# Optimization experiments

Measured on AMD Instinct MI355X. Metric: run time of the kernel, lower is better.

Reference implementation:

```python
import jax, jax.numpy as jnp
import numpy as np

DIM = 1024
N_HEADS = 16
HEAD_DIM = DIM // N_HEADS
B, S = 2, 2048
NEG = -1e9  # additive causal mask value (finite, safe in low precision)


def setup_inputs() -> dict:
    key = jax.random.key(0)
    k_x, k_q, k_k, k_v, k_o = jax.random.split(key, 5)
    x = jax.random.normal(k_x, (B, S, DIM), dtype=jnp.float32)
    # causal additive mask, broadcastable to [B, H, S, S]
    causal = jnp.triu(jnp.ones((S, S), dtype=bool), k=1)
    mask = jnp.where(causal, NEG, 0.0).astype(jnp.float32)[None, None]
    scale = 1.0 / np.sqrt(DIM)
    wq = jax.random.normal(k_q, (DIM, DIM), dtype=jnp.float32) * scale
    wk = jax.random.normal(k_k, (DIM, DIM), dtype=jnp.float32) * scale
    wv = jax.random.normal(k_v, (DIM, DIM), dtype=jnp.float32) * scale
    wo = jax.random.normal(k_o, (DIM, DIM), dtype=jnp.float32) * scale
    return {"x": x, "mask": mask, "wq": wq, "wk": wk, "wv": wv, "wo": wo}


def reference(x, mask, wq, wk, wv, wo):
    bs, seqlen, _ = x.shape
    # nn.Linear(y) = y @ W^T ; weights stored as (out, in)
    q = (x @ wq.T).reshape(bs, seqlen, N_HEADS, HEAD_DIM)
    k = (x @ wk.T).reshape(bs, seqlen, N_HEADS, HEAD_DIM)
    v = (x @ wv.T).reshape(bs, seqlen, N_HEADS, HEAD_DIM)
    # scores: [B, H, S, S] — intentionally materialized, as in the original
    attn = jnp.einsum('bqhd,bkhd->bhqk', q, k) / np.sqrt(HEAD_DIM)
    attn = attn + mask
    attn = jax.nn.softmax(attn, axis=-1)
    out = jnp.einsum('bhqk,bkhd->bqhd', attn, v).reshape(bs, seqlen, DIM)
    return out @ wo.T
```

## Files before the change

### kernel.cpp

```cpp
#include <hip/hip_runtime.h>

typedef __attribute__((ext_vector_type(8))) short bf16x8;
typedef __attribute__((ext_vector_type(4))) float f32x4;
typedef __attribute__((ext_vector_type(16))) float f32x16;
typedef __attribute__((ext_vector_type(4))) unsigned short u16x4;
typedef __attribute__((ext_vector_type(8))) unsigned short u16x8;

#define DIM 1024
#define SEQ 2048
#define NHEAD 16
#define HDIM 64
#define C2 0.18033688011112042f
#define KFIX 8.0f

__device__ __forceinline__ unsigned short f2bf(float f) {
  union { float f; unsigned u; } v; v.f = f;
  unsigned r = v.u + 0x7fffu + ((v.u >> 16) & 1u);
  return (unsigned short)(r >> 16);
}

__device__ __forceinline__ float bf2f(unsigned short s) {
  union { unsigned u; float f; } v; v.u = ((unsigned)s) << 16;
  return v.f;
}

__device__ __forceinline__ void gload_lds16(const void* g, void* l) {
  __builtin_amdgcn_global_load_lds(
      (const __attribute__((address_space(1))) void*)g,
      (__attribute__((address_space(3))) void*)l, 16, 0, 0);
}

__device__ __forceinline__ f32x16 mfma32(bf16x8 a, bf16x8 b, f32x16 c) {
  return __builtin_amdgcn_mfma_f32_32x32x16_bf16(a, b, c, 0, 0, 0);
}

__device__ __forceinline__ unsigned cvtpk(float lo, float hi) {
  unsigned r;
  asm("v_cvt_pk_bf16_f32 %0, %1, %2" : "=v"(r) : "v"(lo), "v"(hi));
  return r;
}

__global__ void f2bf_all(const float* __restrict__ x, const float* __restrict__ wq,
                         const float* __restrict__ wk, const float* __restrict__ wv,
                         const float* __restrict__ wo, unsigned short* __restrict__ xb,
                         unsigned short* __restrict__ wb) {
  int blk = blockIdx.x;
  const float* src;
  unsigned short* dst;
  int rb;
  if (blk < 4096) { src = x; dst = xb; rb = blk; }
  else {
    int w = (blk - 4096) >> 10;
    src = w == 0 ? wq : w == 1 ? wk : w == 2 ? wv : wo;
    dst = wb + (size_t)w * 1048576;
    rb = (blk - 4096) & 1023;
  }
  int i = rb * 256 + threadIdx.x;
  float4 v = ((const float4*)src)[i];
  u16x4 o;
  o[0] = f2bf(v.x); o[1] = f2bf(v.y); o[2] = f2bf(v.z); o[3] = f2bf(v.w);
  ((u16x4*)dst)[i] = o;
}

__global__ __launch_bounds__(256) void gemm3(
    const unsigned short* __restrict__ xb,
    const unsigned short* __restrict__ wb,
    unsigned short* __restrict__ qkv) {
  __shared__ unsigned short As[2][8192];
  __shared__ unsigned short Bs[2][8192];
  const int bz = blockIdx.x;
  const unsigned short *A, *B;
  unsigned short* C;
  int m0, n0, ldc;
  float cscale = 1.0f;
  if (bz < 512) {
    int xcd = bz & 7, inner = bz >> 3;
    int mm = inner & 3, n = (inner >> 2) & 7, w = inner >> 5;
    m0 = (xcd * 4 + mm) * 128; n0 = n * 128;
    A = xb; B = wb + w * 1048576; C = qkv + w * 4194304; ldc = 1024;
    if (w == 0) cscale = C2;
  } else {
    int idx = bz - 512;
    int xcd = idx & 7, inner = idx >> 3;
    int tt = inner & 3, mv = inner >> 2;
    m0 = mv * 128; n0 = (xcd * 4 + tt) * 128;
    A = wb + 2 * 1048576; B = xb; C = qkv + 2 * 4194304; ldc = 4096;
  }
  const int tid = threadIdx.x;
  const int wv = tid >> 6, lane = tid & 63;
  const int g = lane >> 4, l16 = lane & 15;
  const int wm = (wv >> 1) * 64, wn = (wv & 1) * 64;
  f32x4 acc[4][4] = {};

#define GSTAGE(IT, BUF)                                                        \
  {                                                                            \
    const int kt = (IT) * 64;                                                  \
    _Pragma("unroll")                                                          \
    for (int qq = 0; qq < 4; ++qq) {                                           \
      int rbase = wv * 32 + qq * 8;                                            \
      int r = rbase + (lane >> 3);                                             \
      int cs = ((lane & 7) ^ (r & 7)) * 8;                                     \
      gload_lds16(A + (long long)(m0 + r) * 1024 + kt + cs,                    \
                  &As[BUF][rbase * 64]);                                       \
      gload_lds16(B + (long long)(n0 + r) * 1024 + kt + cs,                    \
                  &Bs[BUF][rbase * 64]);                                       \
    }                                                                          \
  }

  GSTAGE(0, 0);
  __syncthreads();

  for (int it = 0; it < 16; ++it) {
    const int buf = it & 1;
    if (it + 1 < 16) GSTAGE(it + 1, buf ^ 1);
#pragma unroll
    for (int ks = 0; ks < 2; ++ks) {
      bf16x8 af[4], bfr[4];
      const int cb = ks * 64 + g * 16;
#pragma unroll
      for (int mf = 0; mf < 4; ++mf) {
        int row = wm + mf * 16 + l16;
        af[mf] = *(const bf16x8*)((const char*)&As[buf][0] + row * 128 + (cb ^ ((row & 7) << 4)));
      }
#pragma unroll
      for (int nf = 0; nf < 4; ++nf) {
        int row = wn + nf * 16 + l16;
        bfr[nf] = *(const bf16x8*)((const char*)&Bs[buf][0] + row * 128 + (cb ^ ((row & 7) << 4)));
      }
#pragma unroll
      for (int mf = 0; mf < 4; ++mf)
#pragma unroll
        for (int nf = 0; nf < 4; ++nf)
          acc[mf][nf] = __builtin_amdgcn_mfma_f32_16x16x32_bf16(
              af[mf], bfr[nf], acc[mf][nf], 0, 0, 0);
    }
    __syncthreads();
  }

#pragma unroll
  for (int mf = 0; mf < 4; ++mf)
#pragma unroll
    for (int nf = 0; nf < 4; ++nf)
#pragma unroll
      for (int r = 0; r < 4; ++r) {
        long long m = m0 + wm + mf * 16 + g * 4 + r;
        long long n = n0 + wn + nf * 16 + l16;
        C[m * ldc + n] = f2bf(acc[mf][nf][r] * cscale);
      }
}

__global__ __launch_bounds__(256) void gemm_out(
    const unsigned short* __restrict__ A,
    const unsigned short* __restrict__ B,
    float* __restrict__ C) {
  __shared__ unsigned short As[2][8192];
  __shared__ unsigned short Bs[2][8192];
  const int tid = threadIdx.x;
  const int wv = tid >> 6, lane = tid & 63;
  const int g = lane >> 4, l16 = lane & 15;
  const int m0 = blockIdx.y * 128, n0 = blockIdx.x * 128;
  const int wm = (wv >> 1) * 64, wn = (wv & 1) * 64;
  f32x4 acc[4][4] = {};

#define OSTAGE(IT, BUF)                                                        \
  {                                                                            \
    const int kt = (IT) * 64;                                                  \
    _Pragma("unroll")                                                          \
    for (int qq = 0; qq < 4; ++qq) {                                           \
      int rbase = wv * 32 + qq * 8;                                            \
      int r = rbase + (lane >> 3);                                             \
      int cs = ((lane & 7) ^ (r & 7)) * 8;                                     \
      gload_lds16(A + (long long)(m0 + r) * 1024 + kt + cs,                    \
                  &As[BUF][rbase * 64]);                                       \
      gload_lds16(B + (long long)(n0 + r) * 1024 + kt + cs,                    \
                  &Bs[BUF][rbase * 64]);                                       \
    }                                                                          \
  }

  OSTAGE(0, 0);
  __syncthreads();

  for (int it = 0; it < 16; ++it) {
    const int buf = it & 1;
    if (it + 1 < 16) OSTAGE(it + 1, buf ^ 1);
#pragma unroll
    for (int ks = 0; ks < 2; ++ks) {
      bf16x8 af[4], bfr[4];
      const int cb = ks * 64 + g * 16;
#pragma unroll
      for (int mf = 0; mf < 4; ++mf) {
        int row = wm + mf * 16 + l16;
        af[mf] = *(const bf16x8*)((const char*)&As[buf][0] + row * 128 + (cb ^ ((row & 7) << 4)));
      }
#pragma unroll
      for (int nf = 0; nf < 4; ++nf) {
        int row = wn + nf * 16 + l16;
        bfr[nf] = *(const bf16x8*)((const char*)&Bs[buf][0] + row * 128 + (cb ^ ((row & 7) << 4)));
      }
#pragma unroll
      for (int mf = 0; mf < 4; ++mf)
#pragma unroll
        for (int nf = 0; nf < 4; ++nf)
          acc[mf][nf] = __builtin_amdgcn_mfma_f32_16x16x32_bf16(
              af[mf], bfr[nf], acc[mf][nf], 0, 0, 0);
    }
    __syncthreads();
  }

#pragma unroll
  for (int mf = 0; mf < 4; ++mf)
#pragma unroll
    for (int nf = 0; nf < 4; ++nf)
#pragma unroll
      for (int r = 0; r < 4; ++r) {
        long long m = m0 + wm + mf * 16 + g * 4 + r;
        long long n = n0 + wn + nf * 16 + l16;
        C[m * 1024 + n] = acc[mf][nf][r];
      }
}

__global__ __launch_bounds__(256, 3) void attn_kernel(
    const unsigned short* __restrict__ Qg,
    const unsigned short* __restrict__ Kg,
    const unsigned short* __restrict__ VTg,
    unsigned short* __restrict__ Og,
    unsigned short* __restrict__ pacc,
    float* __restrict__ pml) {
  __shared__ unsigned short Kls[2][4096];
  __shared__ unsigned short Vls[2][4096];

  const int tid = threadIdx.x;
  const int wv = tid >> 6, lane = tid & 63;
  const int l32 = lane & 31, hi = lane >> 5;
  const int h = blockIdx.y, b = blockIdx.z;

  const int i = blockIdx.x;
  int qt, c, cn;
  if (i < 16)      { qt = 15 - (i >> 2); c = i & 3; cn = 4; }
  else if (i < 28) { int j = i - 16; qt = 11 - j / 3; c = j % 3; cn = 3; }
  else if (i < 36) { int j = i - 28; qt = 7 - ((j >> 1)); c = j & 1; cn = 2; }
  else             { qt = 39 - i; c = 0; cn = 1; }

  const int nt = 2 * qt + 2;
  const int t0 = c * 8;
  const int tb = min(t0 + 8, nt);
  const int tw = min(tb, 2 * qt + (wv >> 1) + 1);

  const int q = qt * 128 + wv * 32 + l32;
  const long long bh = (long long)b * SEQ * DIM + h * HDIM;
  const long long vbase = (long long)h * HDIM * 4096 + b * SEQ;

  const unsigned short* Qrow = Qg + (long long)(b * SEQ + q) * DIM + h * HDIM;
  bf16x8 qf[4];
#pragma unroll
  for (int ds = 0; ds < 4; ++ds)
    qf[ds] = *(const bf16x8*)(Qrow + ds * 16 + hi * 8);

  f32x16 acc0 = {}, acc1 = {};
  float l_run = 0.f;

  const int sr = lane >> 3, sc = lane & 7;
#define STAGE(T, BUF)                                                          \
  {                                                                            \
    const int kv0s = (T) * 64;                                                 \
    _Pragma("unroll")                                                          \
    for (int s = 0; s < 2; ++s) {                                              \
      int jj = wv * 2 + s;                                                     \
      int r = jj * 8 + sr;                                                     \
      int cs = (sc ^ (r & 7)) * 8;                                             \
      gload_lds16(Kg + bh + (long long)(kv0s + r) * DIM + cs,                  \
                  &Kls[BUF][jj * 512]);                                        \
      gload_lds16(VTg + vbase + (long long)r * 4096 + kv0s + cs,               \
                  &Vls[BUF][jj * 512]);                                        \
    }                                                                          \
  }

  STAGE(t0, 0);
  __syncthreads();

  for (int t = t0; t < tb; ++t) {
    const int buf = (t - t0) & 1;
    if (t + 1 < tb) STAGE(t + 1, buf ^ 1);

    if (t < tw) {
      const int kv0 = t * 64;
      f32x16 s0, s1;
#pragma unroll
      for (int r = 0; r < 16; ++r) { s0[r] = -KFIX; s1[r] = -KFIX; }
      __builtin_amdgcn_s_setprio(1);
#pragma unroll
      for (int ds = 0; ds < 4; ++ds) {
        const int cb = (((ds << 1) | hi) ^ (l32 & 7)) * 16;
        bf16x8 k0 = *(const bf16x8*)((const char*)&Kls[buf][0] + l32 * 128 + cb);
        bf16x8 k1 = *(const bf16x8*)((const char*)&Kls[buf][0] + (32 + l32) * 128 + cb);
        s0 = mfma32(k0, qf[ds], s0);
        s1 = mfma32(k1, qf[ds], s1);
      }
      __builtin_amdgcn_s_setprio(0);

      if (kv0 + 64 > q) {
#pragma unroll
        for (int r = 0; r < 16; ++r) {
          int kw = (r & 3) + 8 * (r >> 2) + 4 * hi;
          if (kv0 + kw > q) s0[r] = -1e30f;
          if (kv0 + 32 + kw > q) s1[r] = -1e30f;
        }
      }

      float at[16];
#pragma unroll
      for (int r = 0; r < 16; ++r) {
        float p0 = exp2f(s0[r]);
        float p1 = exp2f(s1[r]);
        s0[r] = p0; s1[r] = p1;
        at[r] = p0 + p1;
      }
#pragma unroll
      for (int off = 8; off; off >>= 1)
#pragma unroll
        for (int i2 = 0; i2 < off; ++i2) at[i2] += at[i2 + off];
      l_run += at[0] + __shfl_xor(at[0], 32);

      __builtin_amdgcn_s_setprio(1);
#pragma unroll
      for (int kks = 0; kks < 4; ++kks) {
        const int base = (kks & 1) * 8;
        unsigned a0, a1, a2, a3;
        if (kks < 2) {
          a0 = cvtpk(s0[base + 0], s0[base + 1]);
          a1 = cvtpk(s0[base + 2], s0[base + 3]);
          a2 = cvtpk(s0[base + 4], s0[base + 5]);
          a3 = cvtpk(s0[base + 6], s0[base + 7]);
        } else {
          a0 = cvtpk(s1[base + 0], s1[base + 1]);
          a1 = cvtpk(s1[base + 2], s1[base + 3]);
          a2 = cvtpk(s1[base + 4], s1[base + 5]);
          a3 = cvtpk(s1[base + 6], s1[base + 7]);
        }
        asm("v_permlane32_swap_b32 %0, %1" : "+v"(a0), "+v"(a2));
        asm("v_permlane32_swap_b32 %0, %1" : "+v"(a1), "+v"(a3));
        union { unsigned u[4]; bf16x8 v; } pf;
        pf.u[0] = a0; pf.u[1] = a1; pf.u[2] = a2; pf.u[3] = a3;
        const int cb = (((kks << 1) | hi) ^ (l32 & 7)) * 16;
        bf16x8 v0 = *(const bf16x8*)((const char*)&Vls[buf][0] + l32 * 128 + cb);
        bf16x8 v1 = *(const bf16x8*)((const char*)&Vls[buf][0] + (32 + l32) * 128 + cb);
        acc0 = mfma32(v0, pf.v, acc0);
        acc1 = mfma32(v1, pf.v, acc1);
      }
      __builtin_amdgcn_s_setprio(0);
    }
    __syncthreads();
  }

  if (cn == 1) {
    const float inv_l = 1.0f / l_run;
    unsigned short* Orow = Og + (long long)(b * SEQ + q) * DIM + h * HDIM;
#pragma unroll
    for (int dblk = 0; dblk < 2; ++dblk) {
#pragma unroll
      for (int g4 = 0; g4 < 4; ++g4) {
        u16x4 o;
#pragma unroll
        for (int jv = 0; jv < 4; ++jv) {
          float v = (dblk ? acc1[g4 * 4 + jv] : acc0[g4 * 4 + jv]) * inv_l;
          o[jv] = f2bf(v);
        }
        *(u16x4*)(Orow + dblk * 32 + 8 * g4 + 4 * hi) = o;
      }
    }
  } else {
    const int sbase = qt < 8 ? 2 * (qt - 4) : qt < 12 ? 8 + 3 * (qt - 8) : 20 + 4 * (qt - 12);
    const int slot = (b * NHEAD + h) * 36 + sbase + c;
    unsigned short* pbase = pacc + (size_t)slot * 8192 + (wv * 32 + l32) * 64;
#pragma unroll
    for (int dblk = 0; dblk < 2; ++dblk) {
#pragma unroll
      for (int g4 = 0; g4 < 4; ++g4) {
        u16x4 o;
#pragma unroll
        for (int jv = 0; jv < 4; ++jv)
          o[jv] = f2bf(dblk ? acc1[g4 * 4 + jv] : acc0[g4 * 4 + jv]);
        *(u16x4*)(pbase + dblk * 32 + 8 * g4 + 4 * hi) = o;
      }
    }
    if (hi == 0) pml[slot * 128 + wv * 32 + l32] = l_run;
  }
}

__global__ __launch_bounds__(256) void attn_merge(
    const unsigned short* __restrict__ pacc,
    const float* __restrict__ pml,
    unsigned short* __restrict__ Og) {
  const int qt = 4 + blockIdx.x;
  const int h = blockIdx.y, b = blockIdx.z;
  const int cn = (qt >> 2) + 1;
  const int sbase = qt < 8 ? 2 * (qt - 4) : qt < 12 ? 8 + 3 * (qt - 8) : 20 + 4 * (qt - 12);
  const int base_slot = (b * NHEAD + h) * 36 + sbase;
  const int t = threadIdx.x;
  const int ql = t >> 1, d0 = (t & 1) * 32;

  float L = 0.f;
#pragma unroll
  for (int cc = 0; cc < 4; ++cc)
    if (cc < cn) L += pml[(base_slot + cc) * 128 + ql];
  const float invL = 1.0f / L;

  float o[32] = {};
#pragma unroll
  for (int cc = 0; cc < 4; ++cc)
    if (cc < cn) {
      const unsigned short* p = pacc + (size_t)(base_slot + cc) * 8192 + ql * 64 + d0;
#pragma unroll
      for (int k = 0; k < 32; k += 8) {
        u16x8 v = *(const u16x8*)(p + k);
#pragma unroll
        for (int jv = 0; jv < 8; ++jv) o[k + jv] += bf2f(v[jv]);
      }
    }

  const int q = qt * 128 + ql;
  unsigned short* orow = Og + (size_t)(b * SEQ + q) * DIM + h * HDIM + d0;
#pragma unroll
  for (int k = 0; k < 32; k += 8) {
    u16x8 ov;
#pragma unroll
    for (int jv = 0; jv < 8; ++jv) ov[jv] = f2bf(o[k + jv] * invL);
    *(u16x8*)(orow + k) = ov;
  }
}

extern "C" void kernel_launch(void* const* d_in, const int* in_sizes, int n_in,
                              void* d_out, int out_size, void* d_ws, size_t ws_size,
                              hipStream_t stream) {
  const float* x   = (const float*)d_in[0];
  const float* wq  = (const float*)d_in[2];
  const float* wk  = (const float*)d_in[3];
  const float* wv_ = (const float*)d_in[4];
  const float* wo  = (const float*)d_in[5];

  unsigned short* xb  = (unsigned short*)d_ws;
  unsigned short* wb  = xb + (size_t)4096 * 1024;
  unsigned short* qkv = wb + (size_t)4 * 1024 * 1024;
  unsigned short* ao  = qkv + (size_t)3 * 4096 * 1024;
  unsigned short* pacc = ao + (size_t)4096 * 1024;
  float* pml = (float*)(pacc + (size_t)1152 * 8192);

  f2bf_all<<<8192, 256, 0, stream>>>(x, wq, wk, wv_, wo, xb, wb);

  gemm3<<<768, 256, 0, stream>>>(xb, wb, qkv);

  attn_kernel<<<dim3(40, 16, 2), 256, 0, stream>>>(
      qkv, qkv + 4194304, qkv + 2 * 4194304, ao, pacc, pml);

  attn_merge<<<dim3(12, 16, 2), 256, 0, stream>>>(pacc, pml, ao);

  gemm_out<<<dim3(8, 32, 1), 256, 0, stream>>>(ao, wb + 3145728, (float*)d_out);
}
```

Baseline: 125.4 us.

## Skip masked 32-key sub-tiles and compute softmax row sums with MFMA

The attention inner loop now processes each 64-key tile as two 32-key halves and skips halves lying entirely above the causal diagonal for each wave. Only the diagonal half gets the masking pass. The exp row sum moves from a VALU reduction plus shuffle into an extra MFMA against a ones vector, and launch bounds go from 3 to 4 waves per SIMD. The KFIX offset is dropped, so the initial score bias becomes zero. This adds one MFMA per slice and may raise register pressure under the tighter occupancy target.

```diff
diff --git a/kernel.cpp b/kernel.cpp
--- a/kernel.cpp
+++ b/kernel.cpp
@@ -11,7 +11,6 @@
 #define NHEAD 16
 #define HDIM 64
 #define C2 0.18033688011112042f
-#define KFIX 8.0f
 
 __device__ __forceinline__ unsigned short f2bf(float f) {
   union { float f; unsigned u; } v; v.f = f;
@@ -219,7 +218,7 @@
       }
 }
 
-__global__ __launch_bounds__(256, 3) void attn_kernel(
+__global__ __launch_bounds__(256, 4) void attn_kernel(
     const unsigned short* __restrict__ Qg,
     const unsigned short* __restrict__ Kg,
     const unsigned short* __restrict__ VTg,
@@ -244,7 +243,7 @@
   const int nt = 2 * qt + 2;
   const int t0 = c * 8;
   const int tb = min(t0 + 8, nt);
-  const int tw = min(tb, 2 * qt + (wv >> 1) + 1);
+  const int umax = 4 * qt + wv;
 
   const int q = qt * 128 + wv * 32 + l32;
   const long long bh = (long long)b * SEQ * DIM + h * HDIM;
@@ -256,8 +255,11 @@
   for (int ds = 0; ds < 4; ++ds)
     qf[ds] = *(const bf16x8*)(Qrow + ds * 16 + hi * 8);
 
-  f32x16 acc0 = {}, acc1 = {};
-  float l_run = 0.f;
+  bf16x8 ones;
+#pragma unroll
+  for (int j = 0; j < 8; ++j) ones[j] = (short)0x3F80;
+
+  f32x16 acc0 = {}, acc1 = {}, lacc = {};
 
   const int sr = lane >> 3, sc = lane & 7;
 #define STAGE(T, BUF)                                                          \
@@ -282,75 +284,59 @@
     const int buf = (t - t0) & 1;
     if (t + 1 < tb) STAGE(t + 1, buf ^ 1);
 
-    if (t < tw) {
-      const int kv0 = t * 64;
-      f32x16 s0, s1;
-#pragma unroll
-      for (int r = 0; r < 16; ++r) { s0[r] = -KFIX; s1[r] = -KFIX; }
-      __builtin_amdgcn_s_setprio(1);
-#pragma unroll
-      for (int ds = 0; ds < 4; ++ds) {
-        const int cb = (((ds << 1) | hi) ^ (l32 & 7)) * 16;
-        bf16x8 k0 = *(const bf16x8*)((const char*)&Kls[buf][0] + l32 * 128 + cb);
-        bf16x8 k1 = *(const bf16x8*)((const char*)&Kls[buf][0] + (32 + l32) * 128 + cb);
-        s0 = mfma32(k0, qf[ds], s0);
-        s1 = mfma32(k1, qf[ds], s1);
-      }
-      __builtin_amdgcn_s_setprio(0);
-
-      if (kv0 + 64 > q) {
-#pragma unroll
-        for (int r = 0; r < 16; ++r) {
-          int kw = (r & 3) + 8 * (r >> 2) + 4 * hi;
-          if (kv0 + kw > q) s0[r] = -1e30f;
-          if (kv0 + 32 + kw > q) s1[r] = -1e30f;
+#pragma unroll
+    for (int s = 0; s < 2; ++s) {
+      const int u = 2 * t + s;
+      if (u <= umax) {
+        f32x16 sv = {};
+        __builtin_amdgcn_s_setprio(1);
+#pragma unroll
+        for (int ds = 0; ds < 4; ++ds) {
+          const int cbk = (((ds << 1) | hi) ^ (l32 & 7)) * 16;
+          bf16x8 kf = *(const bf16x8*)((const char*)&Kls[buf][0] +
+                                       (s * 32 + l32) * 128 + cbk);
+          sv = mfma32(kf, qf[ds], sv);
         }
-      }
-
-      float at[16];
-#pragma unroll
-      for (int r = 0; r < 16; ++r) {
-        float p0 = exp2f(s0[r]);
-        float p1 = exp2f(s1[r]);
-        s0[r] = p0; s1[r] = p1;
-        at[r] = p0 + p1;
-      }
-#pragma unroll
-      for (int off = 8; off; off >>= 1)
-#pragma unroll
-        for (int i2 = 0; i2 < off; ++i2) at[i2] += at[i2 + off];
-      l_run += at[0] + __shfl_xor(at[0], 32);
-
-      __builtin_amdgcn_s_setprio(1);
-#pragma unroll
-      for (int kks = 0; kks < 4; ++kks) {
-        const int base = (kks & 1) * 8;
-        unsigned a0, a1, a2, a3;
-        if (kks < 2) {
-          a0 = cvtpk(s0[base + 0], s0[base + 1]);
-          a1 = cvtpk(s0[base + 2], s0[base + 3]);
-          a2 = cvtpk(s0[base + 4], s0[base + 5]);
-          a3 = cvtpk(s0[base + 6], s0[base + 7]);
-        } else {
-          a0 = cvtpk(s1[base + 0], s1[base + 1]);
-          a1 = cvtpk(s1[base + 2], s1[base + 3]);
-          a2 = cvtpk(s1[base + 4], s1[base + 5]);
-          a3 = cvtpk(s1[base + 6], s1[base + 7]);
+        __builtin_amdgcn_s_setprio(0);
+
+        if (u == umax) {
+#pragma unroll
+          for (int r = 0; r < 16; ++r) {
+            int kw = (r & 3) + 8 * (r >> 2) + 4 * hi;
+            if (kw > l32) sv[r] = -1e30f;
+          }
         }
-        asm("v_permlane32_swap_b32 %0, %1" : "+v"(a0), "+v"(a2));
-        asm("v_permlane32_swap_b32 %0, %1" : "+v"(a1), "+v"(a3));
-        union { unsigned u[4]; bf16x8 v; } pf;
-        pf.u[0] = a0; pf.u[1] = a1; pf.u[2] = a2; pf.u[3] = a3;
-        const int cb = (((kks << 1) | hi) ^ (l32 & 7)) * 16;
-        bf16x8 v0 = *(const bf16x8*)((const char*)&Vls[buf][0] + l32 * 128 + cb);
-        bf16x8 v1 = *(const bf16x8*)((const char*)&Vls[buf][0] + (32 + l32) * 128 + cb);
-        acc0 = mfma32(v0, pf.v, acc0);
-        acc1 = mfma32(v1, pf.v, acc1);
-      }
-      __builtin_amdgcn_s_setprio(0);
+
+#pragma unroll
+        for (int r = 0; r < 16; ++r) sv[r] = exp2f(sv[r]);
+
+        __builtin_amdgcn_s_setprio(1);
+#pragma unroll
+        for (int kk = 0; kk < 2; ++kk) {
+          const int base = kk * 8;
+          unsigned a0 = cvtpk(sv[base + 0], sv[base + 1]);
+          unsigned a1 = cvtpk(sv[base + 2], sv[base + 3]);
+          unsigned a2 = cvtpk(sv[base + 4], sv[base + 5]);
+          unsigned a3 = cvtpk(sv[base + 6], sv[base + 7]);
+          asm("v_permlane32_swap_b32 %0, %1" : "+v"(a0), "+v"(a2));
+          asm("v_permlane32_swap_b32 %0, %1" : "+v"(a1), "+v"(a3));
+          union { unsigned u4[4]; bf16x8 v; } pf;
+          pf.u4[0] = a0; pf.u4[1] = a1; pf.u4[2] = a2; pf.u4[3] = a3;
+          const int slice = 2 * s + kk;
+          const int cbv = (((slice << 1) | hi) ^ (l32 & 7)) * 16;
+          bf16x8 v0 = *(const bf16x8*)((const char*)&Vls[buf][0] + l32 * 128 + cbv);
+          bf16x8 v1 = *(const bf16x8*)((const char*)&Vls[buf][0] + (32 + l32) * 128 + cbv);
+          acc0 = mfma32(v0, pf.v, acc0);
+          acc1 = mfma32(v1, pf.v, acc1);
+          lacc = mfma32(ones, pf.v, lacc);
+        }
+        __builtin_amdgcn_s_setprio(0);
+      }
     }
     __syncthreads();
   }
+
+  const float l_run = lacc[0];
 
   if (cn == 1) {
     const float inv_l = 1.0f / l_run;
```

Result: no change. 125.1 us (-0.3%).
